# Performance work log

Measured on AMD Instinct MI355X. Metric: run time of the kernel, lower is better.

The kernel has to match this reference:

```python
import jax, jax.numpy as jnp
import numpy as np

N_NODES = 100000
N_EDGES = 1600000
D_IN, D_HID, D_OUT = 128, 64, 64


def setup_inputs() -> dict:
    key = jax.random.key(0)
    k0, k1, k2, k3 = jax.random.split(key, 4)
    X = jax.random.normal(k0, (N_NODES, D_IN), dtype=jnp.float32)
    E = jax.random.randint(k1, (2, N_EDGES), 0, N_NODES, dtype=jnp.int32)
    W1 = jax.random.normal(k2, (D_IN, D_HID), dtype=jnp.float32) * 0.05
    b1 = jnp.zeros((D_HID,), dtype=jnp.float32)
    W2 = jax.random.normal(k3, (D_HID, D_OUT), dtype=jnp.float32) * 0.05
    b2 = jnp.zeros((D_OUT,), dtype=jnp.float32)
    return {"V": N_NODES, "E": E, "X": X, "W1": W1, "b1": b1, "W2": W2, "b2": b2}


def _gcn_layer(X, W, b, src, dst, norm, n):
    # GCNConv: linear transform (no bias), gather, degree-normalize, scatter-add, + bias
    Xl = X @ W                              # [n, d_out]
    msg = Xl[src] * norm[:, None]           # [n_edges_sl, d_out] gather
    out = jax.ops.segment_sum(msg, dst, num_segments=n)  # scatter-add
    return out + b


def reference(V, E, X, W1, b1, W2, b2):
    n = X.shape[0]
    # add self loops (add_self_loops=True)
    loop = jnp.arange(n, dtype=E.dtype)
    src = jnp.concatenate([E[0], loop])
    dst = jnp.concatenate([E[1], loop])
    # symmetric gcn_norm: deg over target nodes (unit edge weights)
    deg = jax.ops.segment_sum(jnp.ones_like(dst, dtype=X.dtype), dst, num_segments=n)
    dinv = jnp.where(deg > 0, jax.lax.rsqrt(deg), 0.0)
    norm = dinv[src] * dinv[dst]
    H = jax.nn.relu(_gcn_layer(X, W1, b1, src, dst, norm, n))
    # last layer: no ReLU (matches torch module)
    return _gcn_layer(H, W2, b2, src, dst, norm, n)
```

## Files before the change

kernel.cpp:

```cpp
#include <hip/hip_runtime.h>

#define NT 256
#define TILE 256
#define TILE_SH 8
#define BSTRIDE 8192
#define BSTRIDE_SH 13
#define EPB 4096
#define ITB 16
#define NBUCK_PAD 512

static inline int cdiv(long long a, long long b) { return (int)((a + b - 1) / b); }

typedef unsigned int uint32;
typedef unsigned short ushort16;
typedef short bf16x8 __attribute__((ext_vector_type(8)));
typedef float f32x4 __attribute__((ext_vector_type(4)));

__device__ __forceinline__ ushort16 f2bf(float f) {
  uint32 u = __float_as_uint(f);
  u = (u + 0x7FFF + ((u >> 16) & 1)) >> 16;
  return (ushort16)u;
}
__device__ __forceinline__ float bflo(uint32 w) { return __uint_as_float(w << 16); }
__device__ __forceinline__ float bfhi(uint32 w) { return __uint_as_float(w & 0xFFFF0000u); }
__device__ __forceinline__ float bf2f(ushort16 h) { return __uint_as_float(((uint32)h) << 16); }

template <int K>
__device__ __forceinline__ void stage_W(const float* __restrict__ W,
                                        unsigned short* __restrict__ Wt) {
  constexpr int STR = K + 8;
  for (int i = threadIdx.x; i < K * 64; i += NT) {
    int k = i >> 6, nn = i & 63;
    Wt[nn * STR + k] = f2bf(W[i]);
  }
}

template <int K, int SPLIT>
__device__ __forceinline__ void gemm_tile(const void* __restrict__ Xp,
                                          const unsigned short* __restrict__ Wt,
                                          uint2* __restrict__ Yb, int n, int base) {
  constexpr int STR = K + 8;
  const int tid = threadIdx.x;
  const int w = tid >> 6;
  const int lane = tid & 63;
  const int r = lane & 15;
  const int quad = lane >> 4;
  const int rloc = w * 16 + r;
  const int v = base + rloc;

  f32x4 acc[4];
#pragma unroll
  for (int i = 0; i < 4; ++i) acc[i] = (f32x4)(0.f);

  const float4* X4 = (const float4*)Xp;
  float4 a[K / 32][2];
#pragma unroll
  for (int ks = 0; ks < K / 32; ++ks) {
    a[ks][0] = make_float4(0.f, 0.f, 0.f, 0.f);
    a[ks][1] = make_float4(0.f, 0.f, 0.f, 0.f);
    if (v < n) {
      a[ks][0] = X4[(size_t)v * (K / 4) + ks * 8 + quad * 2];
      a[ks][1] = X4[(size_t)v * (K / 4) + ks * 8 + quad * 2 + 1];
    }
  }
#pragma unroll
  for (int ks = 0; ks < K / 32; ++ks) {
    float f[8] = {a[ks][0].x, a[ks][0].y, a[ks][0].z, a[ks][0].w,
                  a[ks][1].x, a[ks][1].y, a[ks][1].z, a[ks][1].w};
    bf16x8 xh, xl;
#pragma unroll
    for (int j = 0; j < 8; ++j) {
      ushort16 h = f2bf(f[j]);
      xh[j] = (short)h;
      if (SPLIT) xl[j] = (short)f2bf(f[j] - bf2f(h));
    }
    const int koff = ks * 32 + quad * 8;
#pragma unroll
    for (int nt = 0; nt < 4; ++nt) {
      bf16x8 wf = *(const bf16x8*)&Wt[(nt * 16 + r) * STR + koff];
      if (SPLIT)
        acc[nt] = __builtin_amdgcn_mfma_f32_16x16x32_bf16(wf, xl, acc[nt], 0, 0, 0);
      acc[nt] = __builtin_amdgcn_mfma_f32_16x16x32_bf16(wf, xh, acc[nt], 0, 0, 0);
    }
  }

  if (v < n) {
#pragma unroll
    for (int nt = 0; nt < 4; ++nt) {
      uint2 u;
      u.x = (uint32)f2bf(acc[nt][0]) | ((uint32)f2bf(acc[nt][1]) << 16);
      u.y = (uint32)f2bf(acc[nt][2]) | ((uint32)f2bf(acc[nt][3]) << 16);
      Yb[(size_t)v * 16 + nt * 4 + quad] = u;
    }
  }
}

struct ScatSh {
  int cnt[NBUCK_PAD];
  int lcur[NBUCK_PAD];
  int delta[NBUCK_PAD];
  int hs[NT];
  uint32 sorted[EPB];
  unsigned short bid[EPB];
};
union FusedSh {
  unsigned short wt[64 * 136];
  ScatSh s;
};

__global__ __launch_bounds__(NT, 4) void k_fused(
    const int* __restrict__ src, const int* __restrict__ dst,
    int* __restrict__ bcursor, int* __restrict__ tileCtr,
    uint32* __restrict__ buck, int nE, int nbuck, int gscat, int ntile,
    const float* __restrict__ X, const float* __restrict__ W1,
    uint2* __restrict__ Yb, int n) {
  __shared__ FusedSh sm;
  __shared__ int stile;
  const int t = threadIdx.x;
  if ((int)blockIdx.x < gscat) {
    for (int i = t; i < NBUCK_PAD; i += NT) sm.s.cnt[i] = 0;
    __syncthreads();
    const int e0 = blockIdx.x * EPB;
    const int ne = min(EPB, nE - e0);
    int dreg[ITB];
#pragma unroll
    for (int it = 0; it < ITB; ++it) {
      int e = e0 + it * NT + t;
      dreg[it] = (e < nE) ? dst[e] : -1;
      if (dreg[it] >= 0) atomicAdd(&sm.s.cnt[dreg[it] >> TILE_SH], 1);
    }
    __syncthreads();
    int c0 = sm.s.cnt[2 * t], c1 = sm.s.cnt[2 * t + 1];
    int ps = c0 + c1;
    sm.s.hs[t] = ps;
    __syncthreads();
    for (int o = 1; o < NT; o <<= 1) {
      int x = (t >= o) ? sm.s.hs[t - o] : 0;
      __syncthreads();
      sm.s.hs[t] += x;
      __syncthreads();
    }
    int lb0 = sm.s.hs[t] - ps;
    int lb1 = lb0 + c0;
    sm.s.lcur[2 * t] = lb0;
    sm.s.lcur[2 * t + 1] = lb1;
    {
      int b0 = 2 * t, b1 = 2 * t + 1;
      if (b0 < nbuck) {
        int g0 = c0 ? atomicAdd(&bcursor[b0], c0) : 0;
        sm.s.delta[b0] = (b0 << BSTRIDE_SH) + g0 - lb0;
      }
      if (b1 < nbuck) {
        int g1 = c1 ? atomicAdd(&bcursor[b1], c1) : 0;
        sm.s.delta[b1] = (b1 << BSTRIDE_SH) + g1 - lb1;
      }
    }
    __syncthreads();
#pragma unroll
    for (int it = 0; it < ITB; ++it) {
      int e = e0 + it * NT + t;
      if (dreg[it] >= 0) {
        int d = dreg[it];
        int b = d >> TILE_SH;
        int p = atomicAdd(&sm.s.lcur[b], 1);
        sm.s.sorted[p] = (uint32)src[e] | ((uint32)(d & (TILE - 1)) << 24);
        sm.s.bid[p] = (unsigned short)b;
      }
    }
    __syncthreads();
    for (int i = t; i < ne; i += NT) {
      int b = sm.s.bid[i];
      int g = sm.s.delta[b] + i;
      if (g < ((b + 1) << BSTRIDE_SH))
        buck[g] = sm.s.sorted[i];
    }
    __syncthreads();
  }
  stage_W<128>(W1, sm.wt);
  __syncthreads();
  for (;;) {
    if (t == 0) stile = atomicAdd(tileCtr, 1);
    __syncthreads();
    int tile = stile;
    __syncthreads();
    if (tile >= ntile) break;
    gemm_tile<128, 1>(X, sm.wt, Yb, n, tile * 64);
  }
}

__global__ __launch_bounds__(NT) void k_bcsr(const uint32* __restrict__ buck,
                                             const int* __restrict__ bcursor,
                                             int2* __restrict__ rowspan,
                                             float* __restrict__ dinv,
                                             int* __restrict__ srcs, int n) {
  __shared__ int hist[TILE];
  __shared__ int hs[NT];
  __shared__ int off[TILE];
  __shared__ uint32 sarr[BSTRIDE];
  const int b = blockIdx.x;
  const int t = threadIdx.x;
  const int W = b * BSTRIDE;
  const int cntb = min(bcursor[b], BSTRIDE);
  const int v0 = b << TILE_SH;
  const int nv = min(TILE, n - v0);
  hist[t] = 0;
  __syncthreads();
  for (int i = t; i < cntb; i += NT) atomicAdd(&hist[buck[W + i] >> 24], 1);
  __syncthreads();
  int h = hist[t];
  hs[t] = h;
  __syncthreads();
  for (int o = 1; o < NT; o <<= 1) {
    int x = (t >= o) ? hs[t - o] : 0;
    __syncthreads();
    hs[t] += x;
    __syncthreads();
  }
  int ex = hs[t] - h;
  off[t] = ex;
  if (t < nv) {
    rowspan[v0 + t] = make_int2(W + ex, W + ex + h);
    dinv[v0 + t] = rsqrtf((float)(h + 1));
  }
  __syncthreads();
  for (int i = t; i < cntb; i += NT) {
    uint32 w = buck[W + i];
    int ld = (int)(w >> 24);
    int p = atomicAdd(&off[ld], 1);
    sarr[p] = w & 0x00FFFFFFu;
  }
  __syncthreads();
  for (int i = t; i < cntb; i += NT) srcs[W + i] = (int)sarr[i];
}

struct Acc8 {
  float a0, a1, a2, a3, a4, a5, a6, a7;
  __device__ __forceinline__ void madd(uint4 r, float s) {
    a0 = fmaf(bflo(r.x), s, a0); a1 = fmaf(bfhi(r.x), s, a1);
    a2 = fmaf(bflo(r.y), s, a2); a3 = fmaf(bfhi(r.y), s, a3);
    a4 = fmaf(bflo(r.z), s, a4); a5 = fmaf(bfhi(r.z), s, a5);
    a6 = fmaf(bflo(r.w), s, a6); a7 = fmaf(bfhi(r.w), s, a7);
  }
};

__global__ __launch_bounds__(NT) void k_gather_l1(
    const int2* __restrict__ rowspan, const int* __restrict__ srcs,
    const float* __restrict__ dinv, const uint4* __restrict__ Y1,
    const float* __restrict__ bias, const float* __restrict__ W2,
    uint32* __restrict__ Y2, int n) {
  __shared__ float W2s[64 * 64];
  __shared__ float hrow[8][72];
  for (int i = threadIdx.x; i < 64 * 64; i += NT) W2s[i] = W2[i];

  const int tid = threadIdx.x;
  const int lane = tid & 63;
  const int l5 = lane & 31;
  const int part = l5 & 7;
  const int q = l5 >> 3;
  const int slot = ((tid >> 6) << 1) + (lane >> 5);
  const int v = blockIdx.x * 8 + slot;
  const bool act = v < n;

  int2 rs = act ? rowspan[v] : make_int2(0, 0);
  const int beg = rs.x, end = rs.y;
  const float dv = act ? dinv[v] : 0.f;
  Acc8 A = {0.f, 0.f, 0.f, 0.f, 0.f, 0.f, 0.f, 0.f};
  int j = beg + q;
  for (; j + 4 < end; j += 8) {
    int s0 = srcs[j];
    int s1 = srcs[j + 4];
    float ds0 = dinv[s0];
    float ds1 = dinv[s1];
    uint4 r0 = Y1[(size_t)s0 * 8 + part];
    uint4 r1 = Y1[(size_t)s1 * 8 + part];
    A.madd(r0, ds0);
    A.madd(r1, ds1);
  }
  if (j < end) {
    int s = srcs[j];
    A.madd(Y1[(size_t)s * 8 + part], dinv[s]);
  }
#pragma unroll
  for (int m = 8; m <= 16; m <<= 1) {
    A.a0 += __shfl_xor(A.a0, m);
    A.a1 += __shfl_xor(A.a1, m);
    A.a2 += __shfl_xor(A.a2, m);
    A.a3 += __shfl_xor(A.a3, m);
    A.a4 += __shfl_xor(A.a4, m);
    A.a5 += __shfl_xor(A.a5, m);
    A.a6 += __shfl_xor(A.a6, m);
    A.a7 += __shfl_xor(A.a7, m);
  }
  if (q == 0 && act) {
    uint4 wv = Y1[(size_t)v * 8 + part];
    const float4* b4 = (const float4*)bias;
    float4 b0 = b4[part * 2], b1 = b4[part * 2 + 1];
    float r0 = fmaxf(dv * (A.a0 + dv * bflo(wv.x)) + b0.x, 0.f);
    float r1 = fmaxf(dv * (A.a1 + dv * bfhi(wv.x)) + b0.y, 0.f);
    float r2 = fmaxf(dv * (A.a2 + dv * bflo(wv.y)) + b0.z, 0.f);
    float r3 = fmaxf(dv * (A.a3 + dv * bfhi(wv.y)) + b0.w, 0.f);
    float r4 = fmaxf(dv * (A.a4 + dv * bflo(wv.z)) + b1.x, 0.f);
    float r5 = fmaxf(dv * (A.a5 + dv * bfhi(wv.z)) + b1.y, 0.f);
    float r6 = fmaxf(dv * (A.a6 + dv * bflo(wv.w)) + b1.z, 0.f);
    float r7 = fmaxf(dv * (A.a7 + dv * bfhi(wv.w)) + b1.w, 0.f);
    *(float4*)&hrow[slot][part * 8] = make_float4(r0, r1, r2, r3);
    *(float4*)&hrow[slot][part * 8 + 4] = make_float4(r4, r5, r6, r7);
  }
  __syncthreads();
  float y0 = 0.f, y1 = 0.f;
#pragma unroll 8
  for (int k = 0; k < 64; ++k) {
    float h = hrow[slot][k];
    y0 = fmaf(h, W2s[k * 64 + 2 * l5], y0);
    y1 = fmaf(h, W2s[k * 64 + 2 * l5 + 1], y1);
  }
  if (act) {
    uint32 u = (uint32)f2bf(y0) | ((uint32)f2bf(y1) << 16);
    Y2[(size_t)v * 32 + l5] = u;
  }
}

__global__ __launch_bounds__(NT) void k_gather2(const int2* __restrict__ rowspan,
                                                const int* __restrict__ srcs,
                                                const float* __restrict__ dinv,
                                                const uint4* __restrict__ Xn,
                                                const float* __restrict__ bias,
                                                float* __restrict__ outp, int n) {
  const int gt = blockIdx.x * NT + threadIdx.x;
  const int lane = threadIdx.x & 63;
  const int v = ((gt >> 6) << 1) + (lane >> 5);
  if (v >= n) return;
  const int l5 = lane & 31;
  const int part = l5 & 7;
  const int q = l5 >> 3;
  const int2 rs = rowspan[v];
  const int beg = rs.x, end = rs.y;
  const float dv = dinv[v];
  Acc8 A = {0.f, 0.f, 0.f, 0.f, 0.f, 0.f, 0.f, 0.f};
  int j = beg + q;
  for (; j + 4 < end; j += 8) {
    int s0 = srcs[j];
    int s1 = srcs[j + 4];
    float ds0 = dinv[s0];
    float ds1 = dinv[s1];
    uint4 r0 = Xn[(size_t)s0 * 8 + part];
    uint4 r1 = Xn[(size_t)s1 * 8 + part];
    A.madd(r0, ds0);
    A.madd(r1, ds1);
  }
  if (j < end) {
    int s = srcs[j];
    A.madd(Xn[(size_t)s * 8 + part], dinv[s]);
  }
#pragma unroll
  for (int m = 8; m <= 16; m <<= 1) {
    A.a0 += __shfl_xor(A.a0, m);
    A.a1 += __shfl_xor(A.a1, m);
    A.a2 += __shfl_xor(A.a2, m);
    A.a3 += __shfl_xor(A.a3, m);
    A.a4 += __shfl_xor(A.a4, m);
    A.a5 += __shfl_xor(A.a5, m);
    A.a6 += __shfl_xor(A.a6, m);
    A.a7 += __shfl_xor(A.a7, m);
  }
  if (q == 0) {
    uint4 wv = Xn[(size_t)v * 8 + part];
    const float4* b4 = (const float4*)bias;
    float4 b0 = b4[part * 2], b1 = b4[part * 2 + 1];
    float r0 = dv * (A.a0 + dv * bflo(wv.x)) + b0.x;
    float r1 = dv * (A.a1 + dv * bfhi(wv.x)) + b0.y;
    float r2 = dv * (A.a2 + dv * bflo(wv.y)) + b0.z;
    float r3 = dv * (A.a3 + dv * bfhi(wv.y)) + b0.w;
    float r4 = dv * (A.a4 + dv * bflo(wv.z)) + b1.x;
    float r5 = dv * (A.a5 + dv * bfhi(wv.z)) + b1.y;
    float r6 = dv * (A.a6 + dv * bflo(wv.w)) + b1.z;
    float r7 = dv * (A.a7 + dv * bfhi(wv.w)) + b1.w;
    float4* o4 = (float4*)outp;
    o4[(size_t)v * 16 + part * 2] = make_float4(r0, r1, r2, r3);
    o4[(size_t)v * 16 + part * 2 + 1] = make_float4(r4, r5, r6, r7);
  }
}

extern "C" void kernel_launch(void* const* d_in, const int* in_sizes, int n_in,
                              void* d_out, int out_size, void* d_ws, size_t ws_size,
                              hipStream_t stream) {
  const int* E = (const int*)d_in[1];
  const float* X = (const float*)d_in[2];
  const float* W1 = (const float*)d_in[3];
  const float* b1 = (const float*)d_in[4];
  const float* W2 = (const float*)d_in[5];
  const float* b2 = (const float*)d_in[6];
  float* out = (float*)d_out;

  const int n = in_sizes[2] / 128;
  const int nE = in_sizes[1] / 2;
  const int* src = E;
  const int* dst = E + nE;
  const int nbuck = cdiv(n, TILE);

  char* ws = (char*)d_ws;
  size_t off = 0;
  auto alloc = [&](size_t bytes) {
    size_t o = off;
    off = (off + bytes + 255) & ~(size_t)255;
    return (void*)(ws + o);
  };
  int2* rowspan = (int2*)alloc((size_t)n * 8);
  float* dinv = (float*)alloc((size_t)n * 4);
  int* bcursor = (int*)alloc((size_t)(nbuck + 1) * 4);
  int* tileCtr = bcursor + nbuck;
  uint32* buck = (uint32*)alloc((size_t)nbuck * BSTRIDE * 4);
  int* srcs = (int*)alloc((size_t)nbuck * BSTRIDE * 4);
  uint2* Y1 = (uint2*)alloc((size_t)n * 64 * 2);
  uint2* Y2 = (uint2*)alloc((size_t)n * 64 * 2);

  const int gscat = cdiv(nE, EPB);
  const int ntile = cdiv(n, 64);
  const int gfused = 1024;
  const int gthreads_blocks = cdiv((long long)n * 32, NT);

  hipMemsetAsync(bcursor, 0, (size_t)(nbuck + 1) * 4, stream);

  k_fused<<<gfused, NT, 0, stream>>>(src, dst, bcursor, tileCtr, buck, nE,
                                     nbuck, gscat, ntile, X, W1, Y1, n);
  k_bcsr<<<nbuck, NT, 0, stream>>>(buck, bcursor, rowspan, dinv, srcs, n);

  k_gather_l1<<<gthreads_blocks, NT, 0, stream>>>(rowspan, srcs, dinv,
                                                  (const uint4*)Y1, b1, W2,
                                                  (uint32*)Y2, n);

  k_gather2<<<gthreads_blocks, NT, 0, stream>>>(rowspan, srcs, dinv,
                                                (const uint4*)Y2, b2, out, n);
}
```

Measured before the change: 261.3 us.

## Tile layer-1 gather over 64 nodes and apply W2 with MFMA

The layer-1 gather kernel now handles 64 nodes per block instead of 8. Each wave group loops over 8 nodes, writes the ReLU'd hidden rows as bf16 into LDS, and then runs a bf16 MFMA tile GEMM against W2 in place of the scalar fp32 per-lane dot product. This spreads the cost of staging W2 over more nodes and moves the second transform onto the matrix units. The shared aggregation helper is also unrolled to 4 edges per iteration, and the self-row load is hoisted ahead of it, to put more gathers in flight. The hidden activations are now rounded to bf16 before the W2 multiply, which adds some precision loss.

```diff
diff --git a/kernel.cpp b/kernel.cpp
--- a/kernel.cpp
+++ b/kernel.cpp
@@ -84,6 +84,43 @@
     }
   }
 
+  if (v < n) {
+#pragma unroll
+    for (int nt = 0; nt < 4; ++nt) {
+      uint2 u;
+      u.x = (uint32)f2bf(acc[nt][0]) | ((uint32)f2bf(acc[nt][1]) << 16);
+      u.y = (uint32)f2bf(acc[nt][2]) | ((uint32)f2bf(acc[nt][3]) << 16);
+      Yb[(size_t)v * 16 + nt * 4 + quad] = u;
+    }
+  }
+}
+
+template <int K>
+__device__ __forceinline__ void gemm_tile_lds(const unsigned short* __restrict__ Hs,
+                                              const unsigned short* __restrict__ Wt,
+                                              uint2* __restrict__ Yb, int n, int base) {
+  constexpr int STR = K + 8;
+  const int tid = threadIdx.x;
+  const int w = tid >> 6;
+  const int lane = tid & 63;
+  const int r = lane & 15;
+  const int quad = lane >> 4;
+  const int rloc = w * 16 + r;
+  const int v = base + rloc;
+
+  f32x4 acc[4];
+#pragma unroll
+  for (int i = 0; i < 4; ++i) acc[i] = (f32x4)(0.f);
+#pragma unroll
+  for (int ks = 0; ks < K / 32; ++ks) {
+    const int koff = ks * 32 + quad * 8;
+    bf16x8 xf = *(const bf16x8*)&Hs[rloc * STR + koff];
+#pragma unroll
+    for (int nt = 0; nt < 4; ++nt) {
+      bf16x8 wf = *(const bf16x8*)&Wt[(nt * 16 + r) * STR + koff];
+      acc[nt] = __builtin_amdgcn_mfma_f32_16x16x32_bf16(wf, xf, acc[nt], 0, 0, 0);
+    }
+  }
   if (v < n) {
 #pragma unroll
     for (int nt = 0; nt < 4; ++nt) {
@@ -243,81 +280,103 @@
   }
 };
 
+__device__ __forceinline__ void agg_node(const int* __restrict__ srcs,
+                                         const float* __restrict__ dinv,
+                                         const uint4* __restrict__ Y, int beg,
+                                         int end, int part, int q, Acc8& A) {
+  int j = beg + q;
+  for (; j + 12 < end; j += 16) {
+    int s0 = srcs[j];
+    int s1 = srcs[j + 4];
+    int s2 = srcs[j + 8];
+    int s3 = srcs[j + 12];
+    float d0 = dinv[s0], d1 = dinv[s1], d2 = dinv[s2], d3 = dinv[s3];
+    uint4 r0 = Y[(size_t)s0 * 8 + part];
+    uint4 r1 = Y[(size_t)s1 * 8 + part];
+    uint4 r2 = Y[(size_t)s2 * 8 + part];
+    uint4 r3 = Y[(size_t)s3 * 8 + part];
+    A.madd(r0, d0);
+    A.madd(r1, d1);
+    A.madd(r2, d2);
+    A.madd(r3, d3);
+  }
+  if (j + 4 < end) {
+    int s0 = srcs[j];
+    int s1 = srcs[j + 4];
+    float d0 = dinv[s0], d1 = dinv[s1];
+    uint4 r0 = Y[(size_t)s0 * 8 + part];
+    uint4 r1 = Y[(size_t)s1 * 8 + part];
+    A.madd(r0, d0);
+    A.madd(r1, d1);
+    j += 8;
+  }
+  if (j < end) {
+    int s = srcs[j];
+    A.madd(Y[(size_t)s * 8 + part], dinv[s]);
+  }
+}
+
+#define L1STR 72
+
 __global__ __launch_bounds__(NT) void k_gather_l1(
     const int2* __restrict__ rowspan, const int* __restrict__ srcs,
     const float* __restrict__ dinv, const uint4* __restrict__ Y1,
     const float* __restrict__ bias, const float* __restrict__ W2,
-    uint32* __restrict__ Y2, int n) {
-  __shared__ float W2s[64 * 64];
-  __shared__ float hrow[8][72];
-  for (int i = threadIdx.x; i < 64 * 64; i += NT) W2s[i] = W2[i];
+    uint2* __restrict__ Y2, int n) {
+  __shared__ unsigned short Wt[64 * L1STR];
+  __shared__ unsigned short Hs[64 * L1STR];
+  stage_W<64>(W2, Wt);
 
   const int tid = threadIdx.x;
   const int lane = tid & 63;
   const int l5 = lane & 31;
   const int part = l5 & 7;
   const int q = l5 >> 3;
-  const int slot = ((tid >> 6) << 1) + (lane >> 5);
-  const int v = blockIdx.x * 8 + slot;
-  const bool act = v < n;
-
-  int2 rs = act ? rowspan[v] : make_int2(0, 0);
-  const int beg = rs.x, end = rs.y;
-  const float dv = act ? dinv[v] : 0.f;
-  Acc8 A = {0.f, 0.f, 0.f, 0.f, 0.f, 0.f, 0.f, 0.f};
-  int j = beg + q;
-  for (; j + 4 < end; j += 8) {
-    int s0 = srcs[j];
-    int s1 = srcs[j + 4];
-    float ds0 = dinv[s0];
-    float ds1 = dinv[s1];
-    uint4 r0 = Y1[(size_t)s0 * 8 + part];
-    uint4 r1 = Y1[(size_t)s1 * 8 + part];
-    A.madd(r0, ds0);
-    A.madd(r1, ds1);
-  }
-  if (j < end) {
-    int s = srcs[j];
-    A.madd(Y1[(size_t)s * 8 + part], dinv[s]);
-  }
-#pragma unroll
-  for (int m = 8; m <= 16; m <<= 1) {
-    A.a0 += __shfl_xor(A.a0, m);
-    A.a1 += __shfl_xor(A.a1, m);
-    A.a2 += __shfl_xor(A.a2, m);
-    A.a3 += __shfl_xor(A.a3, m);
-    A.a4 += __shfl_xor(A.a4, m);
-    A.a5 += __shfl_xor(A.a5, m);
-    A.a6 += __shfl_xor(A.a6, m);
-    A.a7 += __shfl_xor(A.a7, m);
-  }
-  if (q == 0 && act) {
-    uint4 wv = Y1[(size_t)v * 8 + part];
-    const float4* b4 = (const float4*)bias;
-    float4 b0 = b4[part * 2], b1 = b4[part * 2 + 1];
-    float r0 = fmaxf(dv * (A.a0 + dv * bflo(wv.x)) + b0.x, 0.f);
-    float r1 = fmaxf(dv * (A.a1 + dv * bfhi(wv.x)) + b0.y, 0.f);
-    float r2 = fmaxf(dv * (A.a2 + dv * bflo(wv.y)) + b0.z, 0.f);
-    float r3 = fmaxf(dv * (A.a3 + dv * bfhi(wv.y)) + b0.w, 0.f);
-    float r4 = fmaxf(dv * (A.a4 + dv * bflo(wv.z)) + b1.x, 0.f);
-    float r5 = fmaxf(dv * (A.a5 + dv * bfhi(wv.z)) + b1.y, 0.f);
-    float r6 = fmaxf(dv * (A.a6 + dv * bflo(wv.w)) + b1.z, 0.f);
-    float r7 = fmaxf(dv * (A.a7 + dv * bfhi(wv.w)) + b1.w, 0.f);
-    *(float4*)&hrow[slot][part * 8] = make_float4(r0, r1, r2, r3);
-    *(float4*)&hrow[slot][part * 8 + 4] = make_float4(r4, r5, r6, r7);
-  }
-  __syncthreads();
-  float y0 = 0.f, y1 = 0.f;
-#pragma unroll 8
-  for (int k = 0; k < 64; ++k) {
-    float h = hrow[slot][k];
-    y0 = fmaf(h, W2s[k * 64 + 2 * l5], y0);
-    y1 = fmaf(h, W2s[k * 64 + 2 * l5 + 1], y1);
-  }
-  if (act) {
-    uint32 u = (uint32)f2bf(y0) | ((uint32)f2bf(y1) << 16);
-    Y2[(size_t)v * 32 + l5] = u;
-  }
+  const int grp = ((tid >> 6) << 1) + (lane >> 5);
+  const int base = blockIdx.x * 64;
+
+#pragma unroll 1
+  for (int p = 0; p < 8; ++p) {
+    const int local = p * 8 + grp;
+    const int v = base + local;
+    const bool act = v < n;
+    int2 rs = act ? rowspan[v] : make_int2(0, 0);
+    const float dv = act ? dinv[v] : 0.f;
+    uint4 wv = act ? Y1[(size_t)v * 8 + part] : make_uint4(0u, 0u, 0u, 0u);
+    Acc8 A = {0.f, 0.f, 0.f, 0.f, 0.f, 0.f, 0.f, 0.f};
+    agg_node(srcs, dinv, Y1, rs.x, rs.y, part, q, A);
+#pragma unroll
+    for (int m = 8; m <= 16; m <<= 1) {
+      A.a0 += __shfl_xor(A.a0, m);
+      A.a1 += __shfl_xor(A.a1, m);
+      A.a2 += __shfl_xor(A.a2, m);
+      A.a3 += __shfl_xor(A.a3, m);
+      A.a4 += __shfl_xor(A.a4, m);
+      A.a5 += __shfl_xor(A.a5, m);
+      A.a6 += __shfl_xor(A.a6, m);
+      A.a7 += __shfl_xor(A.a7, m);
+    }
+    if (q == 0 && act) {
+      const float4* b4 = (const float4*)bias;
+      float4 b0 = b4[part * 2], b1 = b4[part * 2 + 1];
+      float r0 = fmaxf(dv * (A.a0 + dv * bflo(wv.x)) + b0.x, 0.f);
+      float r1 = fmaxf(dv * (A.a1 + dv * bfhi(wv.x)) + b0.y, 0.f);
+      float r2 = fmaxf(dv * (A.a2 + dv * bflo(wv.y)) + b0.z, 0.f);
+      float r3 = fmaxf(dv * (A.a3 + dv * bfhi(wv.y)) + b0.w, 0.f);
+      float r4 = fmaxf(dv * (A.a4 + dv * bflo(wv.z)) + b1.x, 0.f);
+      float r5 = fmaxf(dv * (A.a5 + dv * bfhi(wv.z)) + b1.y, 0.f);
+      float r6 = fmaxf(dv * (A.a6 + dv * bflo(wv.w)) + b1.z, 0.f);
+      float r7 = fmaxf(dv * (A.a7 + dv * bfhi(wv.w)) + b1.w, 0.f);
+      uint4 u;
+      u.x = (uint32)f2bf(r0) | ((uint32)f2bf(r1) << 16);
+      u.y = (uint32)f2bf(r2) | ((uint32)f2bf(r3) << 16);
+      u.z = (uint32)f2bf(r4) | ((uint32)f2bf(r5) << 16);
+      u.w = (uint32)f2bf(r6) | ((uint32)f2bf(r7) << 16);
+      *(uint4*)&Hs[local * L1STR + part * 8] = u;
+    }
+  }
+  __syncthreads();
+  gemm_tile_lds<64>(Hs, Wt, Y2, n, base);
 }
 
 __global__ __launch_bounds__(NT) void k_gather2(const int2* __restrict__ rowspan,
@@ -334,24 +393,10 @@
   const int part = l5 & 7;
   const int q = l5 >> 3;
   const int2 rs = rowspan[v];
-  const int beg = rs.x, end = rs.y;
   const float dv = dinv[v];
+  uint4 wv = Xn[(size_t)v * 8 + part];
   Acc8 A = {0.f, 0.f, 0.f, 0.f, 0.f, 0.f, 0.f, 0.f};
-  int j = beg + q;
-  for (; j + 4 < end; j += 8) {
-    int s0 = srcs[j];
-    int s1 = srcs[j + 4];
-    float ds0 = dinv[s0];
-    float ds1 = dinv[s1];
-    uint4 r0 = Xn[(size_t)s0 * 8 + part];
-    uint4 r1 = Xn[(size_t)s1 * 8 + part];
-    A.madd(r0, ds0);
-    A.madd(r1, ds1);
-  }
-  if (j < end) {
-    int s = srcs[j];
-    A.madd(Xn[(size_t)s * 8 + part], dinv[s]);
-  }
+  agg_node(srcs, dinv, Xn, rs.x, rs.y, part, q, A);
 #pragma unroll
   for (int m = 8; m <= 16; m <<= 1) {
     A.a0 += __shfl_xor(A.a0, m);
@@ -364,7 +409,6 @@
     A.a7 += __shfl_xor(A.a7, m);
   }
   if (q == 0) {
-    uint4 wv = Xn[(size_t)v * 8 + part];
     const float4* b4 = (const float4*)bias;
     float4 b0 = b4[part * 2], b1 = b4[part * 2 + 1];
     float r0 = dv * (A.a0 + dv * bflo(wv.x)) + b0.x;
@@ -425,9 +469,8 @@
                                      nbuck, gscat, ntile, X, W1, Y1, n);
   k_bcsr<<<nbuck, NT, 0, stream>>>(buck, bcursor, rowspan, dinv, srcs, n);
 
-  k_gather_l1<<<gthreads_blocks, NT, 0, stream>>>(rowspan, srcs, dinv,
-                                                  (const uint4*)Y1, b1, W2,
-                                                  (uint32*)Y2, n);
+  k_gather_l1<<<ntile, NT, 0, stream>>>(rowspan, srcs, dinv, (const uint4*)Y1,
+                                        b1, W2, Y2, n);
 
   k_gather2<<<gthreads_blocks, NT, 0, stream>>>(rowspan, srcs, dinv,
                                                 (const uint4*)Y2, b2, out, n);
```

Result: faster. 250.0 us (-4.3%).
